# Performance work log

Measured on AMD Instinct MI355X. Metric: run time of the kernel, lower is better.

Reference implementation:

```python
import jax, jax.numpy as jnp
from jax import lax
import numpy as np

OBS_DIM, PROJ, HID, LAT = 128, 64, 256, 24
B, T = 1024, 256


def setup_inputs() -> dict:
    key = jax.random.key(0)
    ks = jax.random.split(key, 10)
    obs = jax.random.normal(ks[0], (B, T, OBS_DIM), dtype=jnp.float32)
    is_init = jax.random.randint(ks[1], (B, T, 1), 0, 2) > 0
    hx = jnp.zeros((B, HID), dtype=jnp.float32)
    # params (fan-in scaled)
    W_in = jax.random.normal(ks[2], (OBS_DIM, PROJ), dtype=jnp.float32) / np.sqrt(OBS_DIM)
    b_in = jnp.zeros((PROJ,), dtype=jnp.float32)
    W_ih = jax.random.normal(ks[3], (PROJ, 3 * HID), dtype=jnp.float32) / np.sqrt(PROJ)
    b_ih = jnp.zeros((3 * HID,), dtype=jnp.float32)
    W_hh = jax.random.normal(ks[4], (HID, 3 * HID), dtype=jnp.float32) / np.sqrt(HID)
    b_hh = jnp.zeros((3 * HID,), dtype=jnp.float32)
    W_out = jax.random.normal(ks[5], (HID, LAT), dtype=jnp.float32) / np.sqrt(HID)
    b_out = jnp.zeros((LAT,), dtype=jnp.float32)
    return dict(obs=obs, is_init=is_init, hx=hx, W_in=W_in, b_in=b_in,
                W_ih=W_ih, b_ih=b_ih, W_hh=W_hh, b_hh=b_hh,
                W_out=W_out, b_out=b_out)


def reference(obs, is_init, hx, W_in, b_in, W_ih, b_ih, W_hh, b_hh, W_out, b_out):
    # input projection: [B,T,OBS] -> [B,T,64]
    x = obs @ W_in + b_in
    # precompute input-side gates once: [B,T,3H]
    gx = jnp.swapaxes(x @ W_ih + b_ih, 0, 1)           # [T,B,3H]
    mask = jnp.swapaxes(is_init.astype(hx.dtype), 0, 1)  # [T,B,1]

    def step(h, inp):
        g, m = inp
        h = h * (1.0 - m)                # episode-reset masking
        gh = h @ W_hh + b_hh             # [B,3H]
        gxr, gxz, gxn = jnp.split(g, 3, axis=-1)
        ghr, ghz, ghn = jnp.split(gh, 3, axis=-1)
        r = jax.nn.sigmoid(gxr + ghr)
        z = jax.nn.sigmoid(gxz + ghz)
        n = jnp.tanh(gxn + r * ghn)
        h_new = (1.0 - z) * n + z * h
        return h_new, h_new

    h_final, ys = lax.scan(step, hx, (gx, mask))
    seq = jnp.swapaxes(ys, 0, 1)         # [B,T,H]
    mish = seq * jnp.tanh(jax.nn.softplus(seq))
    out = mish @ W_out + b_out           # [B,T,LAT]
    return out, h_final
```

## Files before the change

kernel.cpp:

```cpp
#include <hip/hip_runtime.h>
#include <cstdint>
#include <cstddef>

#define OBS_DIMM 128
#define PROJJ    64
#define HIDD     256
#define LATT     24
#define BBATCH   1024
#define TTIME    256
#define NGATE    768
#define MBLK     16
#define CHUNK    64
#define NGROUP   64
#define NCHUNK   4
#define HSTR     264

using bf16x8 = __attribute__((ext_vector_type(8))) short;
using bf16x4 = __attribute__((ext_vector_type(4))) short;
using f32x4  = __attribute__((ext_vector_type(4))) float;

static __device__ __forceinline__ unsigned short f2bf(float f) {
    unsigned u = __builtin_bit_cast(unsigned, f);
    u += 0x7fffu + ((u >> 16) & 1u);
    return (unsigned short)(u >> 16);
}
static __device__ __forceinline__ float bf2f(unsigned short h) {
    return __builtin_bit_cast(float, ((unsigned)h) << 16);
}
static __device__ __forceinline__ float fexp2(float x) { return __builtin_amdgcn_exp2f(x); }
static __device__ __forceinline__ float frcp (float x) { return __builtin_amdgcn_rcpf(x); }
static __device__ __forceinline__ float sigmoid_(float x) { return frcp(1.f + fexp2(-1.44269504f * x)); }
static __device__ __forceinline__ float tanh_(float x)    { return 1.f - 2.f * frcp(fexp2(2.88539008f * x) + 1.f); }
static __device__ __forceinline__ unsigned short mish_bf(float x) {
    float ex = fexp2(1.44269504f * x);
    float t1 = 1.f + ex;
    return f2bf(x * (1.f - 2.f * frcp(t1 * t1 + 1.f)));
}

#define MFMA16(a, b, c) __builtin_amdgcn_mfma_f32_16x16x32_bf16((a), (b), (c), 0, 0, 0)

__global__ void prep_kernel(const float* __restrict__ W_in, const float* __restrict__ b_in,
                            const float* __restrict__ W_ih, const float* __restrict__ b_ih,
                            const float* __restrict__ W_hh, const float* __restrict__ W_out,
                            unsigned short* __restrict__ wsWhh, unsigned short* __restrict__ wsWih,
                            unsigned short* __restrict__ wsWin, unsigned short* __restrict__ wsWo,
                            float* __restrict__ wsBx) {
    int idx = blockIdx.x * 256 + threadIdx.x;
    if (idx < 196608) {
        int k = idx / NGATE, n = idx - k * NGATE;
        int ks = ((k >> 5) << 5) | ((k & 15) << 1) | ((k >> 4) & 1);
        int kt = ks >> 5, q = (ks >> 3) & 3, jj = ks & 7;
        int g = n >> 8, u = n & 255, w = u >> 5, i = (u >> 4) & 1, c16 = u & 15;
        int lane = q * 16 + c16;
        wsWhh[((w * 8 + kt) * 6 + i * 3 + g) * 512 + lane * 8 + jj] = f2bf(W_hh[k * NGATE + n]);
    } else if (idx < 196608 + 49152) {
        int i2 = idx - 196608;
        int k = i2 / NGATE, n = i2 - k * NGATE;
        int kt = k >> 5, q = (k >> 3) & 3, jj = k & 7;
        int g = n >> 8, u = n & 255, w = u >> 5, i = (u >> 4) & 1, c16 = u & 15;
        int lane = q * 16 + c16;
        wsWih[((w * 2 + kt) * 6 + i * 3 + g) * 512 + lane * 8 + jj] = f2bf(W_ih[k * NGATE + n]);
    } else if (idx < 196608 + 49152 + 8192) {
        int i3 = idx - (196608 + 49152);
        int k = i3 >> 6, n = i3 & 63;
        int kt = k >> 5, q = (k >> 3) & 3, jj = k & 7;
        int nt = n >> 4, nl = n & 15;
        wsWin[(kt * 4 + nt) * 512 + (q * 16 + nl) * 8 + jj] = f2bf(W_in[k * PROJJ + n]);
    } else if (idx < 196608 + 49152 + 8192 + 8192) {
        int i4 = idx - (196608 + 49152 + 8192);
        int k = i4 >> 5, n = i4 & 31;
        float s = (n < LATT) ? W_out[k * LATT + n] : 0.f;
        int ks = ((k >> 5) << 5) | ((k & 15) << 1) | ((k >> 4) & 1);
        int kt = ks >> 5, q = (ks >> 3) & 3, jj = ks & 7;
        int nt = n >> 4, nl = n & 15;
        wsWo[(nt * 8 + kt) * 512 + (q * 16 + nl) * 8 + jj] = f2bf(s);
    } else if (idx < 196608 + 49152 + 8192 + 8192 + NGATE) {
        int n = idx - (196608 + 49152 + 8192 + 8192);
        float s = b_ih[n];
        for (int j = 0; j < PROJJ; ++j) s += b_in[j] * W_ih[j * NGATE + n];
        wsBx[n] = s;
    }
}

__global__ __launch_bounds__(256)
void xproj_kernel(const float* __restrict__ obs, const unsigned short* __restrict__ wsWin,
                  unsigned short* __restrict__ xf) {
    __shared__ __align__(16) unsigned short sXP[4][1040];
    const int tid = threadIdx.x, w = tid >> 6, lane = tid & 63, q = lane >> 4, c16 = lane & 15;
    const int tile = blockIdx.x * 4 + w;
    const int g = tile >> 8, t = tile & 255;
    const float* op = obs + ((size_t)(g * 16 + c16) * TTIME + t) * OBS_DIMM + q * 8;
    bf16x8 a[4];
#pragma unroll
    for (int kt = 0; kt < 4; ++kt) {
        float4 u0 = *(const float4*)(op + kt * 32);
        float4 u1 = *(const float4*)(op + kt * 32 + 4);
        bf16x8 v;
        v[0] = (short)f2bf(u0.x); v[1] = (short)f2bf(u0.y);
        v[2] = (short)f2bf(u0.z); v[3] = (short)f2bf(u0.w);
        v[4] = (short)f2bf(u1.x); v[5] = (short)f2bf(u1.y);
        v[6] = (short)f2bf(u1.z); v[7] = (short)f2bf(u1.w);
        a[kt] = v;
    }
    f32x4 acc[4];
#pragma unroll
    for (int nt = 0; nt < 4; ++nt) acc[nt] = (f32x4){0.f, 0.f, 0.f, 0.f};
#pragma unroll
    for (int kt = 0; kt < 4; ++kt)
#pragma unroll
        for (int nt = 0; nt < 4; ++nt)
            acc[nt] = MFMA16(a[kt], *(const bf16x8*)(wsWin + (kt * 4 + nt) * 512 + lane * 8), acc[nt]);
#pragma unroll
    for (int nt = 0; nt < 4; ++nt) {
        int unit = nt * 16 + c16;
        int ktp = unit >> 5, qp = (unit >> 3) & 3, jjp = unit & 7;
#pragma unroll
        for (int r = 0; r < 4; ++r)
            sXP[w][(qp * 16 + q * 4 + r) * 16 + ktp * 8 + jjp] = f2bf(acc[nt][r]);
    }
    __syncthreads();
    unsigned short* dst = xf + (size_t)tile * 1024 + lane * 16;
    *(bf16x8*)dst       = *(const bf16x8*)(sXP[w] + lane * 16);
    *(bf16x8*)(dst + 8) = *(const bf16x8*)(sXP[w] + lane * 16 + 8);
}

__global__ __launch_bounds__(512, 2)
void gru_kernel(const int* __restrict__ is_init, const float* __restrict__ hx,
                const float* __restrict__ b_hh, const float* __restrict__ b_out,
                const unsigned short* __restrict__ wsWhh, const unsigned short* __restrict__ wsWih,
                const unsigned short* __restrict__ wsWo, const float* __restrict__ wsBx,
                const unsigned short* __restrict__ xf,
                float* __restrict__ out, float* __restrict__ hfin) {
    __shared__ __align__(16) unsigned short sWih[49152];
    __shared__ __align__(16) unsigned short sWo[8192];
    __shared__ __align__(16) unsigned short sH[MBLK * HSTR];
    __shared__ __align__(16) unsigned short sM[2][MBLK * HSTR];
    __shared__ __align__(16) float sBias[1056];
    __shared__ int sT;

    const int tid  = threadIdx.x;
    const int w    = tid >> 6;
    const int lane = tid & 63;
    const int q    = lane >> 4;
    const int c16  = lane & 15;
    const int bid  = blockIdx.x;
    const int g    = bid & (NGROUP - 1);
    const int ch   = bid >> 6;
    const int b0   = g * MBLK;
    const int t0   = ch * CHUNK;
    const int tend = t0 + CHUNK;

    const unsigned short* whh_p = wsWhh + (size_t)w * 24576 + lane * 8;
    bf16x8 Whh[48];
#pragma unroll
    for (int f = 0; f < 48; ++f)
        Whh[f] = *(const bf16x8*)(whh_p + (size_t)f * 512);

    {
        const uint4* s1 = (const uint4*)wsWih; uint4* d1 = (uint4*)sWih;
#pragma unroll
        for (int r = 0; r < 12; ++r) d1[r * 512 + tid] = s1[r * 512 + tid];
        const uint4* s3 = (const uint4*)wsWo;  uint4* d3 = (uint4*)sWo;
#pragma unroll
        for (int r = 0; r < 2; ++r) d3[r * 512 + tid] = s3[r * 512 + tid];
    }
    if (tid < 256) {
        sBias[tid]       = wsBx[tid] + b_hh[tid];
        sBias[256 + tid] = wsBx[HIDD + tid] + b_hh[HIDD + tid];
        sBias[512 + tid] = wsBx[2 * HIDD + tid];
        sBias[768 + tid] = b_hh[2 * HIDD + tid];
    } else if (tid < 288) {
        int col = tid - 256;
        sBias[1024 + col] = (col < LATT) ? b_out[col] : 0.f;
    }
    if (tid == 0) sT = (ch == 0) ? 0 : 0x7fffffff;
    __syncthreads();

    if (ch > 0 && tid < MBLK) {
        int b = b0 + tid, fs = 0;
        for (int t = t0 - 1; t > 0; --t) {
            if (is_init[b * TTIME + t] != 0) { fs = t; break; }
        }
        atomicMin(&sT, fs);
    }
    __syncthreads();
    const int tstart = sT;

    {
        int mloc = 0;
#pragma unroll
        for (int r = 0; r < 4; ++r)
            if (is_init[(b0 + q * 4 + r) * TTIME + tstart] != 0) mloc |= 1 << r;
#pragma unroll
        for (int r = 0; r < 4; ++r) {
            float h0v = 0.f, h1v = 0.f;
            if (tstart == 0 && !((mloc >> r) & 1)) {
                const float* hp = hx + (size_t)(b0 + q * 4 + r) * HIDD;
                h0v = hp[(2 * w) * 16 + c16];
                h1v = hp[(2 * w + 1) * 16 + c16];
            }
            ((unsigned*)sH)[(q * 4 + r) * 132 + w * 16 + c16] =
                (unsigned)f2bf(h0v) | ((unsigned)f2bf(h1v) << 16);
        }
    }
    bf16x8 X0, X1;
    {
        const unsigned short* xp = xf + (size_t)(g * 256 + tstart) * 1024 + lane * 16;
        X0 = *(const bf16x8*)xp; X1 = *(const bf16x8*)(xp + 8);
    }
    const unsigned short* wihp = sWih + w * 6144 + lane * 8;
    __syncthreads();

    for (int t = tstart; t < tend; ++t) {
        const bool emit = (t >= t0);
        f32x4 accR[2], accZ[2], accXN[2], accHN[2];
#pragma unroll
        for (int i = 0; i < 2; ++i) {
            int u = (2 * w + i) * 16 + c16;
            float vR = sBias[u], vZ = sBias[256 + u], vX = sBias[512 + u], vH = sBias[768 + u];
            accR[i]  = (f32x4){vR, vR, vR, vR};
            accZ[i]  = (f32x4){vZ, vZ, vZ, vZ};
            accXN[i] = (f32x4){vX, vX, vX, vX};
            accHN[i] = (f32x4){vH, vH, vH, vH};
        }
#pragma unroll
        for (int i = 0; i < 2; ++i) {
            accR[i]  = MFMA16(X0, *(const bf16x8*)(wihp + (i * 3 + 0) * 512), accR[i]);
            accZ[i]  = MFMA16(X0, *(const bf16x8*)(wihp + (i * 3 + 1) * 512), accZ[i]);
            accXN[i] = MFMA16(X0, *(const bf16x8*)(wihp + (i * 3 + 2) * 512), accXN[i]);
            accR[i]  = MFMA16(X1, *(const bf16x8*)(wihp + (6 + i * 3 + 0) * 512), accR[i]);
            accZ[i]  = MFMA16(X1, *(const bf16x8*)(wihp + (6 + i * 3 + 1) * 512), accZ[i]);
            accXN[i] = MFMA16(X1, *(const bf16x8*)(wihp + (6 + i * 3 + 2) * 512), accXN[i]);
        }
        {
            int tn = (t + 1 < TTIME) ? t + 1 : TTIME - 1;
            const unsigned short* xp = xf + (size_t)(g * 256 + tn) * 1024 + lane * 16;
            X0 = *(const bf16x8*)xp; X1 = *(const bf16x8*)(xp + 8);
        }
        int m4 = 0;
        if (t + 1 < tend) {
#pragma unroll
            for (int r = 0; r < 4; ++r)
                if (is_init[(b0 + q * 4 + r) * TTIME + t + 1] != 0) m4 |= 1 << r;
        }
#pragma unroll
        for (int kt = 0; kt < 8; ++kt) {
            bf16x8 a = *(const bf16x8*)(sH + c16 * HSTR + kt * 32 + q * 8);
#pragma unroll
            for (int i = 0; i < 2; ++i) {
                accR[i]  = MFMA16(a, Whh[kt * 6 + i * 3 + 0], accR[i]);
                accZ[i]  = MFMA16(a, Whh[kt * 6 + i * 3 + 1], accZ[i]);
                accHN[i] = MFMA16(a, Whh[kt * 6 + i * 3 + 2], accHN[i]);
            }
        }
        f32x4 oa = (f32x4){0.f, 0.f, 0.f, 0.f};
        const bool doO = ((t & 1) == 0) && (t >= t0 + 2) && (w < 4);
        if (doO) {
            int nt = w & 1;
            float bo = sBias[1024 + nt * 16 + c16];
            oa = (f32x4){bo, bo, bo, bo};
            const unsigned short* smp = sM[w >> 1] + c16 * HSTR + q * 8;
#pragma unroll
            for (int kt = 0; kt < 8; ++kt)
                oa = MFMA16(*(const bf16x8*)(smp + kt * 32),
                            *(const bf16x8*)(sWo + (nt * 8 + kt) * 512 + lane * 8), oa);
        }
        __syncthreads();
        if (doO) {
            int nt = w & 1, col = nt * 16 + c16, tb = t - 2 + (w >> 1);
            if (col < LATT) {
#pragma unroll
                for (int r = 0; r < 4; ++r)
                    out[((size_t)(b0 + q * 4 + r) * TTIME + tb) * LATT + col] = oa[r];
            }
        }
        const int par = t & 1;
#pragma unroll
        for (int r = 0; r < 4; ++r) {
            int bl = q * 4 + r;
            unsigned hpk = ((unsigned*)sH)[bl * 132 + w * 16 + c16];
            float hs0 = bf2f((unsigned short)(hpk & 0xffffu));
            float hs1 = bf2f((unsigned short)(hpk >> 16));
            float rr0 = sigmoid_(accR[0][r]), rr1 = sigmoid_(accR[1][r]);
            float zz0 = sigmoid_(accZ[0][r]), zz1 = sigmoid_(accZ[1][r]);
            float nn0 = tanh_(accXN[0][r] + rr0 * accHN[0][r]);
            float nn1 = tanh_(accXN[1][r] + rr1 * accHN[1][r]);
            float h0 = (1.f - zz0) * nn0 + zz0 * hs0;
            float h1 = (1.f - zz1) * nn1 + zz1 * hs1;
            if (emit)
                ((unsigned*)(sM[par]))[bl * 132 + w * 16 + c16] =
                    (unsigned)mish_bf(h0) | ((unsigned)mish_bf(h1) << 16);
            if ((m4 >> r) & 1) { h0 = 0.f; h1 = 0.f; }
            ((unsigned*)sH)[bl * 132 + w * 16 + c16] =
                (unsigned)f2bf(h0) | ((unsigned)f2bf(h1) << 16);
        }
        __syncthreads();
    }

    if (w < 4) {
        int nt = w & 1;
        float bo = sBias[1024 + nt * 16 + c16];
        f32x4 oa = (f32x4){bo, bo, bo, bo};
        const unsigned short* smp = sM[w >> 1] + c16 * HSTR + q * 8;
#pragma unroll
        for (int kt = 0; kt < 8; ++kt)
            oa = MFMA16(*(const bf16x8*)(smp + kt * 32),
                        *(const bf16x8*)(sWo + (nt * 8 + kt) * 512 + lane * 8), oa);
        int col = nt * 16 + c16, tb = tend - 2 + (w >> 1);
        if (col < LATT) {
#pragma unroll
            for (int r = 0; r < 4; ++r)
                out[((size_t)(b0 + q * 4 + r) * TTIME + tb) * LATT + col] = oa[r];
        }
    }
    if (ch == NCHUNK - 1) {
#pragma unroll
        for (int r = 0; r < 4; ++r) {
            unsigned hpk = ((unsigned*)sH)[(q * 4 + r) * 132 + w * 16 + c16];
            float* hp = hfin + (size_t)(b0 + q * 4 + r) * HIDD;
            hp[(2 * w) * 16 + c16]     = bf2f((unsigned short)(hpk & 0xffffu));
            hp[(2 * w + 1) * 16 + c16] = bf2f((unsigned short)(hpk >> 16));
        }
    }
}

extern "C" void kernel_launch(void* const* d_in, const int* in_sizes, int n_in,
                              void* d_out, int out_size, void* d_ws, size_t ws_size,
                              hipStream_t stream) {
    const float* obs    = (const float*)d_in[0];
    const int*   isini  = (const int*)d_in[1];
    const float* hx     = (const float*)d_in[2];
    const float* W_in   = (const float*)d_in[3];
    const float* b_in   = (const float*)d_in[4];
    const float* W_ih   = (const float*)d_in[5];
    const float* b_ih   = (const float*)d_in[6];
    const float* W_hh   = (const float*)d_in[7];
    const float* b_hh   = (const float*)d_in[8];
    const float* W_out  = (const float*)d_in[9];
    const float* b_out  = (const float*)d_in[10];

    unsigned short* xfbuf = (unsigned short*)d_ws;
    unsigned short* wsWhh = xfbuf + (size_t)BBATCH * TTIME * 64;
    unsigned short* wsWih = wsWhh + 196608;
    unsigned short* wsWin = wsWih + 49152;
    unsigned short* wsWo  = wsWin + 8192;
    float*          wsBx  = (float*)(wsWo + 8192);

    float* outp = (float*)d_out;
    float* hfin = outp + (size_t)BBATCH * TTIME * LATT;

    prep_kernel<<<1027, 256, 0, stream>>>(W_in, b_in, W_ih, b_ih, W_hh, W_out,
                                          wsWhh, wsWih, wsWin, wsWo, wsBx);
    xproj_kernel<<<4096, 256, 0, stream>>>(obs, wsWin, xfbuf);
    gru_kernel<<<256, 512, 0, stream>>>(isini, hx, b_hh, b_out,
                                        wsWhh, wsWih, wsWo, wsBx, xfbuf, outp, hfin);
}
```

Measured before the change: 501.8 us.

## Double-buffer hidden state, triple-buffer mish, one barrier per GRU step

The recurrent loop now keeps the previous hidden state in registers and double-buffers it in shared memory. The mish output buffer is triple-buffered so the output projection can run one step later, spread across all eight waves in rotation. This leaves a single LDS-only barrier per step instead of two __syncthreads. The is_init mask is packed once into shared-memory bitmasks, replacing per-step global loads and the backward scan for the chunk start. The next step's input-gate MFMAs are issued before the barrier, and the prep kernel is rewritten to write its output contiguously.

```diff
diff --git a/kernel.cpp b/kernel.cpp
--- a/kernel.cpp
+++ b/kernel.cpp
@@ -37,6 +37,10 @@
     return f2bf(x * (1.f - 2.f * frcp(t1 * t1 + 1.f)));
 }
 
+static __device__ __forceinline__ void bar_lgkm() {
+    asm volatile("s_waitcnt lgkmcnt(0)\n\ts_barrier" ::: "memory");
+}
+
 #define MFMA16(a, b, c) __builtin_amdgcn_mfma_f32_16x16x32_bf16((a), (b), (c), 0, 0, 0)
 
 __global__ void prep_kernel(const float* __restrict__ W_in, const float* __restrict__ b_in,
@@ -47,35 +51,42 @@
                             float* __restrict__ wsBx) {
     int idx = blockIdx.x * 256 + threadIdx.x;
     if (idx < 196608) {
-        int k = idx / NGATE, n = idx - k * NGATE;
-        int ks = ((k >> 5) << 5) | ((k & 15) << 1) | ((k >> 4) & 1);
-        int kt = ks >> 5, q = (ks >> 3) & 3, jj = ks & 7;
-        int g = n >> 8, u = n & 255, w = u >> 5, i = (u >> 4) & 1, c16 = u & 15;
-        int lane = q * 16 + c16;
-        wsWhh[((w * 8 + kt) * 6 + i * 3 + g) * 512 + lane * 8 + jj] = f2bf(W_hh[k * NGATE + n]);
-    } else if (idx < 196608 + 49152) {
-        int i2 = idx - 196608;
-        int k = i2 / NGATE, n = i2 - k * NGATE;
-        int kt = k >> 5, q = (k >> 3) & 3, jj = k & 7;
-        int g = n >> 8, u = n & 255, w = u >> 5, i = (u >> 4) & 1, c16 = u & 15;
-        int lane = q * 16 + c16;
-        wsWih[((w * 2 + kt) * 6 + i * 3 + g) * 512 + lane * 8 + jj] = f2bf(W_ih[k * NGATE + n]);
-    } else if (idx < 196608 + 49152 + 8192) {
-        int i3 = idx - (196608 + 49152);
-        int k = i3 >> 6, n = i3 & 63;
-        int kt = k >> 5, q = (k >> 3) & 3, jj = k & 7;
-        int nt = n >> 4, nl = n & 15;
-        wsWin[(kt * 4 + nt) * 512 + (q * 16 + nl) * 8 + jj] = f2bf(W_in[k * PROJJ + n]);
-    } else if (idx < 196608 + 49152 + 8192 + 8192) {
-        int i4 = idx - (196608 + 49152 + 8192);
-        int k = i4 >> 5, n = i4 & 31;
-        float s = (n < LATT) ? W_out[k * LATT + n] : 0.f;
-        int ks = ((k >> 5) << 5) | ((k & 15) << 1) | ((k >> 4) & 1);
-        int kt = ks >> 5, q = (ks >> 3) & 3, jj = ks & 7;
-        int nt = n >> 4, nl = n & 15;
-        wsWo[(nt * 8 + kt) * 512 + (q * 16 + nl) * 8 + jj] = f2bf(s);
-    } else if (idx < 196608 + 49152 + 8192 + 8192 + NGATE) {
-        int n = idx - (196608 + 49152 + 8192 + 8192);
+        int f = idx >> 9, rem = idx & 511, l = rem >> 3, jj = rem & 7;
+        int q = l >> 4, c16 = l & 15;
+        int g = f % 3, f2 = f / 3, i = f2 & 1, f3 = f2 >> 1;
+        int kt = f3 & 7, w = f3 >> 3;
+        int s5 = q * 8 + jj;
+        int k = kt * 32 + ((s5 & 1) << 4) + (s5 >> 1);
+        int n = g * 256 + (2 * w + i) * 16 + c16;
+        wsWhh[idx] = f2bf(W_hh[k * NGATE + n]);
+    } else if (idx < 245760) {
+        int d = idx - 196608;
+        int f = d >> 9, rem = d & 511, l = rem >> 3, jj = rem & 7;
+        int q = l >> 4, c16 = l & 15;
+        int g = f % 3, f2 = f / 3, i = f2 & 1, f3 = f2 >> 1;
+        int kt = f3 & 1, w = f3 >> 1;
+        int k = kt * 32 + q * 8 + jj;
+        int n = g * 256 + (2 * w + i) * 16 + c16;
+        wsWih[d] = f2bf(W_ih[k * NGATE + n]);
+    } else if (idx < 253952) {
+        int d = idx - 245760;
+        int f = d >> 9, rem = d & 511, l = rem >> 3, jj = rem & 7;
+        int q = l >> 4, nl = l & 15;
+        int nt = f & 3, kt = f >> 2;
+        int k = kt * 32 + q * 8 + jj;
+        int n = nt * 16 + nl;
+        wsWin[d] = f2bf(W_in[k * PROJJ + n]);
+    } else if (idx < 262144) {
+        int d = idx - 253952;
+        int f = d >> 9, rem = d & 511, l = rem >> 3, jj = rem & 7;
+        int q = l >> 4, nl = l & 15;
+        int kt = f & 7, nt = f >> 3;
+        int s5 = q * 8 + jj;
+        int k = kt * 32 + ((s5 & 1) << 4) + (s5 >> 1);
+        int n = nt * 16 + nl;
+        wsWo[d] = f2bf((n < LATT) ? W_out[k * LATT + n] : 0.f);
+    } else if (idx < 262912) {
+        int n = idx - 262144;
         float s = b_ih[n];
         for (int j = 0; j < PROJJ; ++j) s += b_in[j] * W_ih[j * NGATE + n];
         wsBx[n] = s;
@@ -133,9 +144,10 @@
                 float* __restrict__ out, float* __restrict__ hfin) {
     __shared__ __align__(16) unsigned short sWih[49152];
     __shared__ __align__(16) unsigned short sWo[8192];
-    __shared__ __align__(16) unsigned short sH[MBLK * HSTR];
-    __shared__ __align__(16) unsigned short sM[2][MBLK * HSTR];
+    __shared__ __align__(16) unsigned short sH[2][MBLK * HSTR];
+    __shared__ __align__(16) unsigned short sM[3][MBLK * HSTR];
     __shared__ __align__(16) float sBias[1056];
+    __shared__ unsigned sInit[MBLK][8];
     __shared__ int sT;
 
     const int tid  = threadIdx.x;
@@ -173,35 +185,43 @@
         int col = tid - 256;
         sBias[1024 + col] = (col < LATT) ? b_out[col] : 0.f;
     }
+    if (tid < 128) {
+        int b = tid >> 3, wd = tid & 7;
+        unsigned m = 0;
+        const int* ip = is_init + (size_t)(b0 + b) * TTIME + wd * 32;
+#pragma unroll
+        for (int j = 0; j < 32; ++j) m |= (ip[j] != 0 ? 1u : 0u) << j;
+        sInit[b][wd] = m;
+    }
     if (tid == 0) sT = (ch == 0) ? 0 : 0x7fffffff;
     __syncthreads();
 
     if (ch > 0 && tid < MBLK) {
-        int b = b0 + tid, fs = 0;
-        for (int t = t0 - 1; t > 0; --t) {
-            if (is_init[b * TTIME + t] != 0) { fs = t; break; }
+        int fs = 0;
+        for (int wi = (t0 >> 5) - 1; wi >= 0; --wi) {
+            unsigned m = sInit[tid][wi];
+            if (wi == 0) m &= ~1u;
+            if (m) { fs = wi * 32 + 31 - __builtin_clz(m); break; }
         }
         atomicMin(&sT, fs);
     }
     __syncthreads();
     const int tstart = sT;
 
-    {
-        int mloc = 0;
-#pragma unroll
-        for (int r = 0; r < 4; ++r)
-            if (is_init[(b0 + q * 4 + r) * TTIME + tstart] != 0) mloc |= 1 << r;
-#pragma unroll
-        for (int r = 0; r < 4; ++r) {
-            float h0v = 0.f, h1v = 0.f;
-            if (tstart == 0 && !((mloc >> r) & 1)) {
-                const float* hp = hx + (size_t)(b0 + q * 4 + r) * HIDD;
-                h0v = hp[(2 * w) * 16 + c16];
-                h1v = hp[(2 * w + 1) * 16 + c16];
-            }
-            ((unsigned*)sH)[(q * 4 + r) * 132 + w * 16 + c16] =
-                (unsigned)f2bf(h0v) | ((unsigned)f2bf(h1v) << 16);
-        }
+    unsigned hReg[4];
+#pragma unroll
+    for (int r = 0; r < 4; ++r) {
+        int b = q * 4 + r;
+        unsigned rbit = (sInit[b][tstart >> 5] >> (tstart & 31)) & 1u;
+        float h0v = 0.f, h1v = 0.f;
+        if (tstart == 0 && !rbit) {
+            const float* hp = hx + (size_t)(b0 + b) * HIDD;
+            h0v = hp[2 * w * 16 + c16];
+            h1v = hp[(2 * w + 1) * 16 + c16];
+        }
+        unsigned pk = (unsigned)f2bf(h0v) | ((unsigned)f2bf(h1v) << 16);
+        hReg[r] = pk;
+        ((unsigned*)sH[0])[b * 132 + w * 16 + c16] = pk;
     }
     bf16x8 X0, X1;
     {
@@ -209,11 +229,15 @@
         X0 = *(const bf16x8*)xp; X1 = *(const bf16x8*)(xp + 8);
     }
     const unsigned short* wihp = sWih + w * 6144 + lane * 8;
+    unsigned short* sHr = sH[0];
+    unsigned short* sHw = sH[1];
+    unsigned short* pWm = sM[tstart % 3];
+    unsigned short* pR1 = sM[(tstart + 2) % 3];
+    unsigned short* pR2 = sM[(tstart + 1) % 3];
     __syncthreads();
 
-    for (int t = tstart; t < tend; ++t) {
-        const bool emit = (t >= t0);
-        f32x4 accR[2], accZ[2], accXN[2], accHN[2];
+    f32x4 accR[2], accZ[2], accXN[2], accHN[2];
+    auto accfill = [&]() {
 #pragma unroll
         for (int i = 0; i < 2; ++i) {
             int u = (2 * w + i) * 16 + c16;
@@ -222,9 +246,6 @@
             accZ[i]  = (f32x4){vZ, vZ, vZ, vZ};
             accXN[i] = (f32x4){vX, vX, vX, vX};
             accHN[i] = (f32x4){vH, vH, vH, vH};
-        }
-#pragma unroll
-        for (int i = 0; i < 2; ++i) {
             accR[i]  = MFMA16(X0, *(const bf16x8*)(wihp + (i * 3 + 0) * 512), accR[i]);
             accZ[i]  = MFMA16(X0, *(const bf16x8*)(wihp + (i * 3 + 1) * 512), accZ[i]);
             accXN[i] = MFMA16(X0, *(const bf16x8*)(wihp + (i * 3 + 2) * 512), accXN[i]);
@@ -232,20 +253,18 @@
             accZ[i]  = MFMA16(X1, *(const bf16x8*)(wihp + (6 + i * 3 + 1) * 512), accZ[i]);
             accXN[i] = MFMA16(X1, *(const bf16x8*)(wihp + (6 + i * 3 + 2) * 512), accXN[i]);
         }
+    };
+    accfill();
+
+    for (int t = tstart; t < tend; ++t) {
         {
             int tn = (t + 1 < TTIME) ? t + 1 : TTIME - 1;
             const unsigned short* xp = xf + (size_t)(g * 256 + tn) * 1024 + lane * 16;
             X0 = *(const bf16x8*)xp; X1 = *(const bf16x8*)(xp + 8);
         }
-        int m4 = 0;
-        if (t + 1 < tend) {
-#pragma unroll
-            for (int r = 0; r < 4; ++r)
-                if (is_init[(b0 + q * 4 + r) * TTIME + t + 1] != 0) m4 |= 1 << r;
-        }
 #pragma unroll
         for (int kt = 0; kt < 8; ++kt) {
-            bf16x8 a = *(const bf16x8*)(sH + c16 * HSTR + kt * 32 + q * 8);
+            bf16x8 a = *(const bf16x8*)(sHr + c16 * HSTR + kt * 32 + q * 8);
 #pragma unroll
             for (int i = 0; i < 2; ++i) {
                 accR[i]  = MFMA16(a, Whh[kt * 6 + i * 3 + 0], accR[i]);
@@ -253,34 +272,31 @@
                 accHN[i] = MFMA16(a, Whh[kt * 6 + i * 3 + 2], accHN[i]);
             }
         }
-        f32x4 oa = (f32x4){0.f, 0.f, 0.f, 0.f};
-        const bool doO = ((t & 1) == 0) && (t >= t0 + 2) && (w < 4);
+        f32x4 oa;
+        const bool doO = (t >= t0 + 2) && ((w >> 1) == (t & 3));
         if (doO) {
             int nt = w & 1;
             float bo = sBias[1024 + nt * 16 + c16];
             oa = (f32x4){bo, bo, bo, bo};
-            const unsigned short* smp = sM[w >> 1] + c16 * HSTR + q * 8;
+            const unsigned short* smp = pR2 + c16 * HSTR + q * 8;
 #pragma unroll
             for (int kt = 0; kt < 8; ++kt)
                 oa = MFMA16(*(const bf16x8*)(smp + kt * 32),
                             *(const bf16x8*)(sWo + (nt * 8 + kt) * 512 + lane * 8), oa);
         }
-        __syncthreads();
-        if (doO) {
-            int nt = w & 1, col = nt * 16 + c16, tb = t - 2 + (w >> 1);
-            if (col < LATT) {
-#pragma unroll
-                for (int r = 0; r < 4; ++r)
-                    out[((size_t)(b0 + q * 4 + r) * TTIME + tb) * LATT + col] = oa[r];
-            }
-        }
-        const int par = t & 1;
+        int m4 = 0;
+        if (t + 1 < tend) {
+            int wd = (t + 1) >> 5, bt = (t + 1) & 31;
+#pragma unroll
+            for (int r = 0; r < 4; ++r)
+                m4 |= (int)((sInit[q * 4 + r][wd] >> bt) & 1u) << r;
+        }
+        const bool emit = (t >= t0);
 #pragma unroll
         for (int r = 0; r < 4; ++r) {
             int bl = q * 4 + r;
-            unsigned hpk = ((unsigned*)sH)[bl * 132 + w * 16 + c16];
-            float hs0 = bf2f((unsigned short)(hpk & 0xffffu));
-            float hs1 = bf2f((unsigned short)(hpk >> 16));
+            float hs0 = bf2f((unsigned short)(hReg[r] & 0xffffu));
+            float hs1 = bf2f((unsigned short)(hReg[r] >> 16));
             float rr0 = sigmoid_(accR[0][r]), rr1 = sigmoid_(accR[1][r]);
             float zz0 = sigmoid_(accZ[0][r]), zz1 = sigmoid_(accZ[1][r]);
             float nn0 = tanh_(accXN[0][r] + rr0 * accHN[0][r]);
@@ -288,38 +304,51 @@
             float h0 = (1.f - zz0) * nn0 + zz0 * hs0;
             float h1 = (1.f - zz1) * nn1 + zz1 * hs1;
             if (emit)
-                ((unsigned*)(sM[par]))[bl * 132 + w * 16 + c16] =
+                ((unsigned*)pWm)[bl * 132 + w * 16 + c16] =
                     (unsigned)mish_bf(h0) | ((unsigned)mish_bf(h1) << 16);
             if ((m4 >> r) & 1) { h0 = 0.f; h1 = 0.f; }
-            ((unsigned*)sH)[bl * 132 + w * 16 + c16] =
-                (unsigned)f2bf(h0) | ((unsigned)f2bf(h1) << 16);
-        }
-        __syncthreads();
+            unsigned pk = (unsigned)f2bf(h0) | ((unsigned)f2bf(h1) << 16);
+            hReg[r] = pk;
+            ((unsigned*)sHw)[bl * 132 + w * 16 + c16] = pk;
+        }
+        if (doO) {
+            int nt = w & 1, col = nt * 16 + c16, tb = t - 2;
+            if (col < LATT) {
+#pragma unroll
+                for (int r = 0; r < 4; ++r)
+                    out[((size_t)(b0 + q * 4 + r) * TTIME + tb) * LATT + col] = oa[r];
+            }
+        }
+        if (t + 1 < tend) accfill();
+        bar_lgkm();
+        { unsigned short* tp = sHr; sHr = sHw; sHw = tp; }
+        { unsigned short* tp = pWm; pWm = pR2; pR2 = pR1; pR1 = tp; }
     }
 
     if (w < 4) {
         int nt = w & 1;
+        unsigned short* pR = (w < 2) ? pR2 : pR1;
+        int tb = (w < 2) ? tend - 2 : tend - 1;
         float bo = sBias[1024 + nt * 16 + c16];
-        f32x4 oa = (f32x4){bo, bo, bo, bo};
-        const unsigned short* smp = sM[w >> 1] + c16 * HSTR + q * 8;
+        f32x4 oa2 = (f32x4){bo, bo, bo, bo};
+        const unsigned short* smp = pR + c16 * HSTR + q * 8;
 #pragma unroll
         for (int kt = 0; kt < 8; ++kt)
-            oa = MFMA16(*(const bf16x8*)(smp + kt * 32),
-                        *(const bf16x8*)(sWo + (nt * 8 + kt) * 512 + lane * 8), oa);
-        int col = nt * 16 + c16, tb = tend - 2 + (w >> 1);
+            oa2 = MFMA16(*(const bf16x8*)(smp + kt * 32),
+                         *(const bf16x8*)(sWo + (nt * 8 + kt) * 512 + lane * 8), oa2);
+        int col = nt * 16 + c16;
         if (col < LATT) {
 #pragma unroll
             for (int r = 0; r < 4; ++r)
-                out[((size_t)(b0 + q * 4 + r) * TTIME + tb) * LATT + col] = oa[r];
+                out[((size_t)(b0 + q * 4 + r) * TTIME + tb) * LATT + col] = oa2[r];
         }
     }
     if (ch == NCHUNK - 1) {
 #pragma unroll
         for (int r = 0; r < 4; ++r) {
-            unsigned hpk = ((unsigned*)sH)[(q * 4 + r) * 132 + w * 16 + c16];
             float* hp = hfin + (size_t)(b0 + q * 4 + r) * HIDD;
-            hp[(2 * w) * 16 + c16]     = bf2f((unsigned short)(hpk & 0xffffu));
-            hp[(2 * w + 1) * 16 + c16] = bf2f((unsigned short)(hpk >> 16));
+            hp[2 * w * 16 + c16]       = bf2f((unsigned short)(hReg[r] & 0xffffu));
+            hp[(2 * w + 1) * 16 + c16] = bf2f((unsigned short)(hReg[r] >> 16));
         }
     }
 }
```

New measurement: 491.4 us. 2.1% less time.
